# Kernel optimization log

Hardware: AMD Instinct MI355X
Metric: run time of the kernel (lower is better)

## Reference

```python
import jax, jax.numpy as jnp
import numpy as np
import math

B, L, D, H = 4, 1024, 1024, 16
HD = D // H

def setup_inputs() -> dict:
    rng = jax.random.key(0)
    ks = jax.random.split(rng, 11)
    def lin(k):
        # orthogonal-ish init not needed for numerics; normal scaled like torch default
        return jax.random.normal(k, (D, D), dtype=jnp.float32) * 0.02
    return {
        'key':   jax.random.normal(ks[0], (B, L, D), dtype=jnp.float32),
        'value': jax.random.normal(ks[1], (B, L, D), dtype=jnp.float32),
        'query': jax.random.normal(ks[2], (B, L, D), dtype=jnp.float32),
        'Wk': lin(ks[3]), 'bk': jnp.zeros((D,), jnp.float32),
        'Wq': lin(ks[4]), 'bq': jnp.zeros((D,), jnp.float32),
        'Wv': lin(ks[5]), 'bv': jnp.zeros((D,), jnp.float32),
        'Wp': lin(ks[6]), 'bp': jnp.zeros((D,), jnp.float32),
    }

def reference(key, value, query, Wk, bk, Wq, bq, Wv, bv, Wp, bp):
    # linear projections (torch Linear: x @ W.T + b)
    k = (key   @ Wk.T + bk).reshape(B, L, H, HD).transpose(0, 2, 1, 3)  # [B,H,L,hd]
    q = (query @ Wq.T + bq).reshape(B, L, H, HD).transpose(0, 2, 1, 3)
    v = (value @ Wv.T + bv).reshape(B, L, H, HD).transpose(0, 2, 1, 3)
    att = jnp.einsum('bhqd,bhkd->bhqk', q, k) * (1.0 / math.sqrt(HD))  # [B,H,L,L]
    causal = jnp.tril(jnp.ones((L, L), dtype=bool))
    att = jnp.where(causal[None, None], att, -jnp.inf)
    att = jax.nn.softmax(att, axis=-1)
    y = jnp.einsum('bhqk,bhkd->bhqd', att, v)  # [B,H,L,hd]
    y = y.transpose(0, 2, 1, 3).reshape(B, L, D)
    return y @ Wp.T + bp
```

## Files before the change

### kernel.cpp

```cpp
#include <hip/hip_runtime.h>

typedef unsigned short u16;
typedef __attribute__((ext_vector_type(8))) short bf16x8;
typedef __attribute__((ext_vector_type(4))) float f32x4;
typedef __attribute__((ext_vector_type(4))) unsigned short u16x4;

#define MFMA16 __builtin_amdgcn_mfma_f32_16x16x32_bf16

__device__ inline u16 f2bf(float f) {
    union { float f; unsigned u; } v; v.f = f;
    return (u16)((v.u + 0x8000u) >> 16);
}

__device__ inline void gld16(const u16* g, u16* l) {
    __builtin_amdgcn_global_load_lds(
        (const __attribute__((address_space(1))) unsigned int*)g,
        (__attribute__((address_space(3))) unsigned int*)l, 16, 0, 0);
}

struct CvtArgs { const float* src[7]; u16* dst[7]; };

__global__ __launch_bounds__(256) void cvt_kernel(CvtArgs a) {
    const int bid = blockIdx.x;
    int z, local;
    if (bid < 6144) { z = bid >> 11; local = bid & 2047; }
    else            { z = 3 + ((bid - 6144) >> 9); local = (bid - 6144) & 511; }
    const size_t i = ((size_t)local * 256 + threadIdx.x) * 8;
    const float* s = a.src[z];
    float4 v0 = *(const float4*)(s + i);
    float4 v1 = *(const float4*)(s + i + 4);
    union { u16 h[8]; bf16x8 v; } o;
    o.h[0] = f2bf(v0.x); o.h[1] = f2bf(v0.y); o.h[2] = f2bf(v0.z); o.h[3] = f2bf(v0.w);
    o.h[4] = f2bf(v1.x); o.h[5] = f2bf(v1.y); o.h[6] = f2bf(v1.z); o.h[7] = f2bf(v1.w);
    *(bf16x8*)(a.dst[z] + i) = o.v;
}

struct GemmArgs { const u16* A; const u16* W; const float* bias; void* out; int epi; };
struct Gemm3Args { GemmArgs g[3]; };

__global__ __launch_bounds__(256, 3) void gemm_qkv(Gemm3Args ga) {
    __shared__ u16 lA[128 * 64];
    __shared__ u16 lB[128 * 64];
    const GemmArgs g = ga.g[blockIdx.z];
    const int t = threadIdx.x, wave = t >> 6, lane = t & 63;
    const int quad = lane >> 4, l16 = lane & 15;
    const int bid = blockIdx.x;
    const int mtile = (bid & 7) * 4 + (bid >> 6);
    const int ntile = (bid >> 3) & 7;
    const int rowsA = mtile * 128, rowsB = ntile * 128;
    const int wm = (wave >> 1) * 64, wn = (wave & 1) * 64;
    const u16* A = g.A; const u16* W = g.W;

    f32x4 acc[4][4] = {};

    for (int kb = 0; kb < 1024; kb += 64) {
#pragma unroll
        for (int i = 0; i < 4; i++) {
            int u = (i * 4 + wave) * 64 + lane;
            int row = u >> 3, cu = (u & 7) ^ (row & 7);
            gld16(A + (size_t)(rowsA + row) * 1024 + kb + cu * 8, lA + u * 8);
        }
#pragma unroll
        for (int i = 0; i < 4; i++) {
            int u = (i * 4 + wave) * 64 + lane;
            int row = u >> 3, cu = (u & 7) ^ (row & 7);
            gld16(W + (size_t)(rowsB + row) * 1024 + kb + cu * 8, lB + u * 8);
        }
        __syncthreads();

        bf16x8 af[4][2], bfr[4][2];
#pragma unroll
        for (int mi = 0; mi < 4; mi++) {
            int row = wm + mi * 16 + l16;
#pragma unroll
            for (int kr = 0; kr < 2; kr++)
                af[mi][kr] = *(const bf16x8*)(lA + row * 64 + (((kr * 4 + quad) ^ (row & 7)) * 8));
        }
#pragma unroll
        for (int ni = 0; ni < 4; ni++) {
            int row = wn + ni * 16 + l16;
#pragma unroll
            for (int kr = 0; kr < 2; kr++)
                bfr[ni][kr] = *(const bf16x8*)(lB + row * 64 + (((kr * 4 + quad) ^ (row & 7)) * 8));
        }
#pragma unroll
        for (int mi = 0; mi < 4; mi++)
#pragma unroll
            for (int ni = 0; ni < 4; ni++) {
                acc[mi][ni] = MFMA16(af[mi][0], bfr[ni][0], acc[mi][ni], 0, 0, 0);
                acc[mi][ni] = MFMA16(af[mi][1], bfr[ni][1], acc[mi][ni], 0, 0, 0);
            }
        __syncthreads();
    }

    const int epi = g.epi;
#pragma unroll
    for (int ni = 0; ni < 4; ni++) {
        const int ncol = rowsB + wn + ni * 16 + l16;
        const float bv = g.bias[ncol];
        const int h = ncol >> 6, hd = ncol & 63;
#pragma unroll
        for (int mi = 0; mi < 4; mi++) {
            const int mrow0 = rowsA + wm + mi * 16 + quad * 4;
            const int b = mrow0 >> 10, l0 = mrow0 & 1023;
            if (epi == 0) {
#pragma unroll
                for (int r = 0; r < 4; r++)
                    ((u16*)g.out)[((size_t)(b * 16 + h) * 1024 + l0 + r) * 64 + hd] =
                        f2bf(acc[mi][ni][r] + bv);
            } else {
                u16x4 pk;
#pragma unroll
                for (int r = 0; r < 4; r++) pk[r] = f2bf(acc[mi][ni][r] + bv);
                *(u16x4*)((u16*)g.out + ((size_t)(b * 16 + h) * 64 + hd) * 1024 + l0) = pk;
            }
        }
    }
}

__global__ __launch_bounds__(256, 2) void gemm_p(const u16* __restrict__ A,
                                                 const u16* __restrict__ W,
                                                 const float* __restrict__ bias,
                                                 float* __restrict__ out)
{
    __shared__ u16 lA[128 * 64];
    __shared__ u16 lB[64 * 64];
    const int t = threadIdx.x, wave = t >> 6, lane = t & 63;
    const int quad = lane >> 4, l16 = lane & 15;
    const int bid = blockIdx.x;
    const int mtile = (bid & 7) * 4 + (bid >> 7);
    const int ntile = (bid >> 3) & 15;
    const int rowsA = mtile * 128, rowsB = ntile * 64;
    const int wm = (wave >> 1) * 64, wn = (wave & 1) * 32;

    f32x4 acc[4][2] = {};

    for (int kb = 0; kb < 1024; kb += 64) {
#pragma unroll
        for (int i = 0; i < 4; i++) {
            int u = (i * 4 + wave) * 64 + lane;
            int row = u >> 3, cu = (u & 7) ^ (row & 7);
            gld16(A + (size_t)(rowsA + row) * 1024 + kb + cu * 8, lA + u * 8);
        }
#pragma unroll
        for (int i = 0; i < 2; i++) {
            int u = (i * 4 + wave) * 64 + lane;
            int row = u >> 3, cu = (u & 7) ^ (row & 7);
            gld16(W + (size_t)(rowsB + row) * 1024 + kb + cu * 8, lB + u * 8);
        }
        __syncthreads();

        bf16x8 af[4][2], bfr[2][2];
#pragma unroll
        for (int mi = 0; mi < 4; mi++) {
            int row = wm + mi * 16 + l16;
#pragma unroll
            for (int kr = 0; kr < 2; kr++)
                af[mi][kr] = *(const bf16x8*)(lA + row * 64 + (((kr * 4 + quad) ^ (row & 7)) * 8));
        }
#pragma unroll
        for (int ni = 0; ni < 2; ni++) {
            int row = wn + ni * 16 + l16;
#pragma unroll
            for (int kr = 0; kr < 2; kr++)
                bfr[ni][kr] = *(const bf16x8*)(lB + row * 64 + (((kr * 4 + quad) ^ (row & 7)) * 8));
        }
#pragma unroll
        for (int mi = 0; mi < 4; mi++)
#pragma unroll
            for (int ni = 0; ni < 2; ni++) {
                acc[mi][ni] = MFMA16(af[mi][0], bfr[ni][0], acc[mi][ni], 0, 0, 0);
                acc[mi][ni] = MFMA16(af[mi][1], bfr[ni][1], acc[mi][ni], 0, 0, 0);
            }
        __syncthreads();
    }

#pragma unroll
    for (int ni = 0; ni < 2; ni++) {
        const int ncol = rowsB + wn + ni * 16 + l16;
        const float bv = bias[ncol];
#pragma unroll
        for (int mi = 0; mi < 4; mi++) {
            const int mrow0 = rowsA + wm + mi * 16 + quad * 4;
#pragma unroll
            for (int r = 0; r < 4; r++)
                out[(size_t)(mrow0 + r) * 1024 + ncol] = acc[mi][ni][r] + bv;
        }
    }
}

__global__ __launch_bounds__(256, 2) void attn_kernel(const u16* __restrict__ qh,
                                                      const u16* __restrict__ kh,
                                                      const u16* __restrict__ vhT,
                                                      u16* __restrict__ y)
{
    __shared__ u16 sK[2][64 * 64];
    __shared__ u16 sVT[2][64 * 64];
    __shared__ u16 sP[4 * 16 * 72];

    const int t = threadIdx.x, wave = t >> 6, lane = t & 63;
    const int quad = lane >> 4, l16 = lane & 15;
    const int bid = blockIdx.x;
    const int bh = (bid & 7) * 8 + ((bid >> 3) & 7);
    const int pr = bid >> 6;
    const int qbaseA = pr * 64 + wave * 16;
    const int qbaseB = (15 - pr) * 64 + wave * 16;
    const size_t base = (size_t)bh * 1024 * 64;
    const float e2 = 0.18033688f;

    bf16x8 aqA[2], aqB[2];
#pragma unroll
    for (int kr = 0; kr < 2; kr++) {
        aqA[kr] = *(const bf16x8*)(qh + base + (size_t)(qbaseA + l16) * 64 + kr * 32 + quad * 8);
        aqB[kr] = *(const bf16x8*)(qh + base + (size_t)(qbaseB + l16) * 64 + kr * 32 + quad * 8);
    }

    bf16x8 ones;
#pragma unroll
    for (int j = 0; j < 8; j++) ones[j] = (short)0x3F80;

    f32x4 oA[4] = {}, oB[4] = {};
    f32x4 laccA = {}, laccB = {};
    u16* pw = sP + wave * 16 * 72;

    auto STAGE = [&](int kb, int b) {
        const int krow0 = kb * 64;
#pragma unroll
        for (int i = 0; i < 2; i++) {
            int u = (i * 4 + wave) * 64 + lane;
            int row = u >> 3, cu = (u & 7) ^ (row & 7);
            gld16(kh + base + (size_t)(krow0 + row) * 64 + cu * 8, &sK[b][0] + u * 8);
        }
#pragma unroll
        for (int i = 0; i < 2; i++) {
            int u = (i * 4 + wave) * 64 + lane;
            int row = u >> 3, cu = (u & 7) ^ (row & 7);
            gld16(vhT + ((size_t)(bh * 64 + row)) * 1024 + krow0 + cu * 8, &sVT[b][0] + u * 8);
        }
    };

    STAGE(0, 0);
    __syncthreads();

    const int last = 15 - pr;
    int cur = 0;
    for (int kb = 0; kb <= last; kb++) {
        if (kb < last) STAGE(kb + 1, cur ^ 1);
        const int krow0 = kb * 64;
        const bool actA = (kb <= pr);
        const u16* sKc = sK[cur];
        const u16* sVc = sVT[cur];

        bf16x8 bk[4][2];
#pragma unroll
        for (int kc = 0; kc < 4; kc++) {
            int row = kc * 16 + l16;
#pragma unroll
            for (int kr = 0; kr < 2; kr++)
                bk[kc][kr] = *(const bf16x8*)(sKc + row * 64 + (((kr * 4 + quad) ^ (row & 7)) * 8));
        }
        f32x4 scA[4], scB[4];
        __builtin_amdgcn_s_setprio(1);
#pragma unroll
        for (int kc = 0; kc < 4; kc++) {
            f32x4 z = {};
            z = MFMA16(aqB[0], bk[kc][0], z, 0, 0, 0);
            z = MFMA16(aqB[1], bk[kc][1], z, 0, 0, 0);
            scB[kc] = z;
        }
        if (actA) {
#pragma unroll
            for (int kc = 0; kc < 4; kc++) {
                f32x4 z = {};
                z = MFMA16(aqA[0], bk[kc][0], z, 0, 0, 0);
                z = MFMA16(aqA[1], bk[kc][1], z, 0, 0, 0);
                scA[kc] = z;
            }
        }
        __builtin_amdgcn_s_setprio(0);

        bf16x8 apA0, apA1, apB0, apB1;
        if (actA) {
            const bool dmA = (krow0 + 63 > qbaseA);
#pragma unroll
            for (int kc = 0; kc < 4; kc++)
#pragma unroll
                for (int r = 0; r < 4; r++) {
                    float xv = fminf(scA[kc][r] * e2, 43.f);
                    float pv = exp2f(xv);
                    if (dmA) {
                        int kcol = krow0 + kc * 16 + l16;
                        int qrow = qbaseA + quad * 4 + r;
                        if (kcol > qrow) pv = 0.f;
                    }
                    pw[(quad * 4 + r) * 72 + kc * 16 + l16] = f2bf(pv);
                }
            apA0 = *(const bf16x8*)(pw + l16 * 72 + quad * 8);
            apA1 = *(const bf16x8*)(pw + l16 * 72 + 32 + quad * 8);
        }
        {
            const bool dmB = (krow0 + 63 > qbaseB);
#pragma unroll
            for (int kc = 0; kc < 4; kc++)
#pragma unroll
                for (int r = 0; r < 4; r++) {
                    float xv = fminf(scB[kc][r] * e2, 43.f);
                    float pv = exp2f(xv);
                    if (dmB) {
                        int kcol = krow0 + kc * 16 + l16;
                        int qrow = qbaseB + quad * 4 + r;
                        if (kcol > qrow) pv = 0.f;
                    }
                    pw[(quad * 4 + r) * 72 + kc * 16 + l16] = f2bf(pv);
                }
            apB0 = *(const bf16x8*)(pw + l16 * 72 + quad * 8);
            apB1 = *(const bf16x8*)(pw + l16 * 72 + 32 + quad * 8);
        }

        bf16x8 bv[4][2];
#pragma unroll
        for (int nt = 0; nt < 4; nt++) {
            int row = nt * 16 + l16;
#pragma unroll
            for (int kr = 0; kr < 2; kr++)
                bv[nt][kr] = *(const bf16x8*)(sVc + row * 64 + (((kr * 4 + quad) ^ (row & 7)) * 8));
        }
        __builtin_amdgcn_s_setprio(1);
#pragma unroll
        for (int nt = 0; nt < 4; nt++) {
            oB[nt] = MFMA16(apB0, bv[nt][0], oB[nt], 0, 0, 0);
            oB[nt] = MFMA16(apB1, bv[nt][1], oB[nt], 0, 0, 0);
        }
        laccB = MFMA16(apB0, ones, laccB, 0, 0, 0);
        laccB = MFMA16(apB1, ones, laccB, 0, 0, 0);
        if (actA) {
#pragma unroll
            for (int nt = 0; nt < 4; nt++) {
                oA[nt] = MFMA16(apA0, bv[nt][0], oA[nt], 0, 0, 0);
                oA[nt] = MFMA16(apA1, bv[nt][1], oA[nt], 0, 0, 0);
            }
            laccA = MFMA16(apA0, ones, laccA, 0, 0, 0);
            laccA = MFMA16(apA1, ones, laccA, 0, 0, 0);
        }
        __builtin_amdgcn_s_setprio(0);
        __syncthreads();
        cur ^= 1;
    }

    const int b = bh >> 4, h = bh & 15;
#pragma unroll
    for (int nt = 0; nt < 4; nt++)
#pragma unroll
        for (int r = 0; r < 4; r++) {
            int d = nt * 16 + l16;
            int qrA = qbaseA + quad * 4 + r;
            int qrB = qbaseB + quad * 4 + r;
            y[(size_t)(b * 1024 + qrA) * 1024 + h * 64 + d] = f2bf(oA[nt][r] / laccA[r]);
            y[(size_t)(b * 1024 + qrB) * 1024 + h * 64 + d] = f2bf(oB[nt][r] / laccB[r]);
        }
}

extern "C" void kernel_launch(void* const* d_in, const int* in_sizes, int n_in,
                              void* d_out, int out_size, void* d_ws, size_t ws_size,
                              hipStream_t stream)
{
    const float* key   = (const float*)d_in[0];
    const float* value = (const float*)d_in[1];
    const float* query = (const float*)d_in[2];
    const float* Wk = (const float*)d_in[3];
    const float* bk = (const float*)d_in[4];
    const float* Wq = (const float*)d_in[5];
    const float* bq = (const float*)d_in[6];
    const float* Wv = (const float*)d_in[7];
    const float* bv = (const float*)d_in[8];
    const float* Wp = (const float*)d_in[9];
    const float* bp = (const float*)d_in[10];

    char* ws = (char*)d_ws;
    u16* xq  = (u16*)(ws + (size_t)( 0 << 20));
    u16* xk  = (u16*)(ws + (size_t)( 8 << 20));
    u16* xv  = (u16*)(ws + (size_t)(16 << 20));
    u16* wqb = (u16*)(ws + (size_t)(24 << 20));
    u16* wkb = (u16*)(ws + (size_t)(26 << 20));
    u16* wvb = (u16*)(ws + (size_t)(28 << 20));
    u16* wpb = (u16*)(ws + (size_t)(30 << 20));
    u16* qh  = (u16*)(ws + (size_t)(32 << 20));
    u16* kh  = (u16*)(ws + (size_t)(40 << 20));
    u16* vhT = (u16*)(ws + (size_t)(48 << 20));
    u16* y   = xq;

    CvtArgs ca;
    ca.src[0] = query; ca.dst[0] = xq;
    ca.src[1] = key;   ca.dst[1] = xk;
    ca.src[2] = value; ca.dst[2] = xv;
    ca.src[3] = Wq;    ca.dst[3] = wqb;
    ca.src[4] = Wk;    ca.dst[4] = wkb;
    ca.src[5] = Wv;    ca.dst[5] = wvb;
    ca.src[6] = Wp;    ca.dst[6] = wpb;
    hipLaunchKernelGGL(cvt_kernel, dim3(8192), dim3(256), 0, stream, ca);

    Gemm3Args g3;
    g3.g[0] = GemmArgs{xq, wqb, bq, (void*)qh,  0};
    g3.g[1] = GemmArgs{xk, wkb, bk, (void*)kh,  0};
    g3.g[2] = GemmArgs{xv, wvb, bv, (void*)vhT, 2};
    hipLaunchKernelGGL(gemm_qkv, dim3(256, 1, 3), dim3(256), 0, stream, g3);

    hipLaunchKernelGGL(attn_kernel, dim3(512), dim3(256), 0, stream, qh, kh, vhT, y);

    hipLaunchKernelGGL(gemm_p, dim3(512), dim3(256), 0, stream, y, wpb, bp, (float*)d_out);
}
```

Measured before the change: 191.4 us.

## Keep attention probabilities in registers via transposed QK^T MFMA layout

Swaps the MFMA operand order for the score computation so each lane holds the S^T fragment whose layout matches the A-operand of the PV MFMA. Probabilities are packed to bf16 in registers with v_cvt_pk_bf16_f32 instead of round-tripping through a per-wave LDS buffer. The V fragment loads are split into two 8-byte reads to match the new k-index permutation. This removes LDS writes and reads plus the scalar bf16 conversion in the softmax path, at the cost of more LDS read instructions for V and changed mask indexing.

```diff
diff --git a/kernel.cpp b/kernel.cpp
--- a/kernel.cpp
+++ b/kernel.cpp
@@ -10,6 +10,12 @@
 __device__ inline u16 f2bf(float f) {
     union { float f; unsigned u; } v; v.f = f;
     return (u16)((v.u + 0x8000u) >> 16);
+}
+
+__device__ inline unsigned cvtpk(float lo, float hi) {
+    unsigned r;
+    asm("v_cvt_pk_bf16_f32 %0, %1, %2" : "=v"(r) : "v"(lo), "v"(hi));
+    return r;
 }
 
 __device__ inline void gld16(const u16* g, u16* l) {
@@ -196,7 +202,6 @@
 {
     __shared__ u16 sK[2][64 * 64];
     __shared__ u16 sVT[2][64 * 64];
-    __shared__ u16 sP[4 * 16 * 72];
 
     const int t = threadIdx.x, wave = t >> 6, lane = t & 63;
     const int quad = lane >> 4, l16 = lane & 15;
@@ -221,7 +226,6 @@
 
     f32x4 oA[4] = {}, oB[4] = {};
     f32x4 laccA = {}, laccB = {};
-    u16* pw = sP + wave * 16 * 72;
 
     auto STAGE = [&](int kb, int b) {
         const int krow0 = kb * 64;
@@ -264,24 +268,25 @@
 #pragma unroll
         for (int kc = 0; kc < 4; kc++) {
             f32x4 z = {};
-            z = MFMA16(aqB[0], bk[kc][0], z, 0, 0, 0);
-            z = MFMA16(aqB[1], bk[kc][1], z, 0, 0, 0);
+            z = MFMA16(bk[kc][0], aqB[0], z, 0, 0, 0);
+            z = MFMA16(bk[kc][1], aqB[1], z, 0, 0, 0);
             scB[kc] = z;
         }
         if (actA) {
 #pragma unroll
             for (int kc = 0; kc < 4; kc++) {
                 f32x4 z = {};
-                z = MFMA16(aqA[0], bk[kc][0], z, 0, 0, 0);
-                z = MFMA16(aqA[1], bk[kc][1], z, 0, 0, 0);
+                z = MFMA16(bk[kc][0], aqA[0], z, 0, 0, 0);
+                z = MFMA16(bk[kc][1], aqA[1], z, 0, 0, 0);
                 scA[kc] = z;
             }
         }
         __builtin_amdgcn_s_setprio(0);
 
-        bf16x8 apA0, apA1, apB0, apB1;
+        bf16x8 apA[2], apB[2];
         if (actA) {
             const bool dmA = (krow0 + 63 > qbaseA);
+            const int qrowA = qbaseA + l16;
 #pragma unroll
             for (int kc = 0; kc < 4; kc++)
 #pragma unroll
@@ -289,17 +294,26 @@
                     float xv = fminf(scA[kc][r] * e2, 43.f);
                     float pv = exp2f(xv);
                     if (dmA) {
-                        int kcol = krow0 + kc * 16 + l16;
-                        int qrow = qbaseA + quad * 4 + r;
-                        if (kcol > qrow) pv = 0.f;
+                        int kcol = krow0 + kc * 16 + quad * 4 + r;
+                        if (kcol > qrowA) pv = 0.f;
                     }
-                    pw[(quad * 4 + r) * 72 + kc * 16 + l16] = f2bf(pv);
+                    scA[kc][r] = pv;
                 }
-            apA0 = *(const bf16x8*)(pw + l16 * 72 + quad * 8);
-            apA1 = *(const bf16x8*)(pw + l16 * 72 + 32 + quad * 8);
+#pragma unroll
+            for (int kr = 0; kr < 2; kr++) {
+                union { unsigned w[4]; bf16x8 v; } u;
+#pragma unroll
+                for (int w = 0; w < 4; w++) {
+                    int kc = kr * 2 + (w >> 1);
+                    int r0 = (w & 1) * 2;
+                    u.w[w] = cvtpk(scA[kc][r0], scA[kc][r0 + 1]);
+                }
+                apA[kr] = u.v;
+            }
         }
         {
             const bool dmB = (krow0 + 63 > qbaseB);
+            const int qrowB = qbaseB + l16;
 #pragma unroll
             for (int kc = 0; kc < 4; kc++)
 #pragma unroll
@@ -307,40 +321,56 @@
                     float xv = fminf(scB[kc][r] * e2, 43.f);
                     float pv = exp2f(xv);
                     if (dmB) {
-                        int kcol = krow0 + kc * 16 + l16;
-                        int qrow = qbaseB + quad * 4 + r;
-                        if (kcol > qrow) pv = 0.f;
+                        int kcol = krow0 + kc * 16 + quad * 4 + r;
+                        if (kcol > qrowB) pv = 0.f;
                     }
-                    pw[(quad * 4 + r) * 72 + kc * 16 + l16] = f2bf(pv);
+                    scB[kc][r] = pv;
                 }
-            apB0 = *(const bf16x8*)(pw + l16 * 72 + quad * 8);
-            apB1 = *(const bf16x8*)(pw + l16 * 72 + 32 + quad * 8);
+#pragma unroll
+            for (int kr = 0; kr < 2; kr++) {
+                union { unsigned w[4]; bf16x8 v; } u;
+#pragma unroll
+                for (int w = 0; w < 4; w++) {
+                    int kc = kr * 2 + (w >> 1);
+                    int r0 = (w & 1) * 2;
+                    u.w[w] = cvtpk(scB[kc][r0], scB[kc][r0 + 1]);
+                }
+                apB[kr] = u.v;
+            }
         }
 
         bf16x8 bv[4][2];
 #pragma unroll
         for (int nt = 0; nt < 4; nt++) {
             int row = nt * 16 + l16;
-#pragma unroll
-            for (int kr = 0; kr < 2; kr++)
-                bv[nt][kr] = *(const bf16x8*)(sVc + row * 64 + (((kr * 4 + quad) ^ (row & 7)) * 8));
-        }
+            const u16* rp = sVc + row * 64;
+#pragma unroll
+            for (int kr = 0; kr < 2; kr++) {
+                int g0 = kr * 4 + (quad >> 1);
+                int off = (quad & 1) * 4;
+                union { u16x4 q[2]; bf16x8 v; } u;
+                u.q[0] = *(const u16x4*)(rp + ((g0 ^ (row & 7)) * 8 + off));
+                u.q[1] = *(const u16x4*)(rp + (((g0 + 2) ^ (row & 7)) * 8 + off));
+                bv[nt][kr] = u.v;
+            }
+        }
+
         __builtin_amdgcn_s_setprio(1);
 #pragma unroll
         for (int nt = 0; nt < 4; nt++) {
-            oB[nt] = MFMA16(apB0, bv[nt][0], oB[nt], 0, 0, 0);
-            oB[nt] = MFMA16(apB1, bv[nt][1], oB[nt], 0, 0, 0);
-        }
-        laccB = MFMA16(apB0, ones, laccB, 0, 0, 0);
-        laccB = MFMA16(apB1, ones, laccB, 0, 0, 0);
+            oB[nt] = MFMA16(apB[0], bv[nt][0], oB[nt], 0, 0, 0);
+            oB[nt] = MFMA16(apB[1], bv[nt][1], oB[nt], 0, 0, 0);
+        }
+        laccB = MFMA16(apB[0], ones, laccB, 0, 0, 0);
+        laccB = MFMA16(apB[1], ones, laccB, 0, 0, 0);
         if (actA) {
 #pragma unroll
             for (int nt = 0; nt < 4; nt++) {
-                oA[nt] = MFMA16(apA0, bv[nt][0], oA[nt], 0, 0, 0);
-                oA[nt] = MFMA16(apA1, bv[nt][1], oA[nt], 0, 0, 0);
-            }
-            laccA = MFMA16(apA0, ones, laccA, 0, 0, 0);
-            laccA = MFMA16(apA1, ones, laccA, 0, 0, 0);
+                oA[nt] = MFMA16(apA[0], bv[nt][0], oA[nt], 0, 0, 0);
+                oA[nt] = MFMA16(apA[1], bv[nt][1], oA[nt], 0, 0, 0);
+            }
+            laccA = MFMA16(apA[0], ones, laccA, 0, 0, 0);
+            laccA = MFMA16(apA[1], ones, laccA, 0, 0, 0);
         }
         __builtin_amdgcn_s_setprio(0);
         __syncthreads();
```

Result: slower. 197.2 us (+3.0%).
